# Performance work log

Hardware: AMD Instinct MI355X
Metric: run time of the kernel (lower is better)

## Reference

```python
import math
import jax, jax.numpy as jnp
import numpy as np

C = 1024
H = 16
HD = C // H
T = 2048
B = 2
EPS = 1e-5


def setup_inputs() -> dict:
    key = jax.random.key(0)
    ks = jax.random.split(key, 8)
    s = 0.02
    return {
        "x": jax.random.normal(ks[0], (B, T, C), dtype=jnp.float32),
        "ln1_g": jnp.ones((C,), jnp.float32),
        "ln1_b": jnp.zeros((C,), jnp.float32),
        "w_attn": jax.random.normal(ks[1], (C, 3 * C), dtype=jnp.float32) * s,
        "b_attn": jnp.zeros((3 * C,), jnp.float32),
        "w_proj": jax.random.normal(ks[2], (C, C), dtype=jnp.float32) * s,
        "b_proj": jnp.zeros((C,), jnp.float32),
        "ln2_g": jnp.ones((C,), jnp.float32),
        "ln2_b": jnp.zeros((C,), jnp.float32),
        "w_fc": jax.random.normal(ks[3], (C, 4 * C), dtype=jnp.float32) * s,
        "b_fc": jnp.zeros((4 * C,), jnp.float32),
        "w_fc2": jax.random.normal(ks[4], (4 * C, C), dtype=jnp.float32) * s,
        "b_fc2": jnp.zeros((C,), jnp.float32),
    }


def _layernorm(x, g, b):
    mu = jnp.mean(x, axis=-1, keepdims=True)
    var = jnp.mean((x - mu) ** 2, axis=-1, keepdims=True)
    return (x - mu) * jax.lax.rsqrt(var + EPS) * g + b


def _attention(x, w_attn, b_attn, w_proj, b_proj):
    Bb, Tt, Cc = x.shape
    qkv = x @ w_attn + b_attn  # (B,T,3C)
    q, k, v = jnp.split(qkv, 3, axis=-1)
    # (B,H,T,HD)
    q = q.reshape(Bb, Tt, H, HD).transpose(0, 2, 1, 3)
    k = k.reshape(Bb, Tt, H, HD).transpose(0, 2, 1, 3)
    v = v.reshape(Bb, Tt, H, HD).transpose(0, 2, 1, 3)
    scale = 1.0 / math.sqrt(HD)
    attn = jnp.einsum("bhqd,bhkd->bhqk", q, k) * scale
    causal = jnp.tril(jnp.ones((Tt, Tt), dtype=bool))
    attn = jnp.where(causal[None, None], attn, -jnp.inf)
    attn = jax.nn.softmax(attn, axis=-1)
    out = jnp.einsum("bhqk,bhkd->bhqd", attn, v)
    out = out.transpose(0, 2, 1, 3).reshape(Bb, Tt, Cc)
    return out @ w_proj + b_proj


def _mlp(x, w_fc, b_fc, w_fc2, b_fc2):
    h = jax.nn.gelu(x @ w_fc + b_fc, approximate=True)
    return h @ w_fc2 + b_fc2


def reference(x, ln1_g, ln1_b, w_attn, b_attn, w_proj, b_proj,
              ln2_g, ln2_b, w_fc, b_fc, w_fc2, b_fc2):
    x = x + _attention(_layernorm(x, ln1_g, ln1_b), w_attn, b_attn, w_proj, b_proj)
    x = x + _mlp(_layernorm(x, ln2_g, ln2_b), w_fc, b_fc, w_fc2, b_fc2)
    return x
```

## Files before the change

kernel.cpp:

```cpp
#include <hip/hip_runtime.h>
#include <math.h>

#define TB 2
#define TT 2048
#define TC 1024
#define TH 16
#define THD 64
#define TM (TB*TT)
#define NQT 32

typedef __bf16 bf16x8 __attribute__((ext_vector_type(8)));
typedef float f32x4 __attribute__((ext_vector_type(4)));
typedef unsigned short u16x8 __attribute__((ext_vector_type(8)));
typedef unsigned short u16x4 __attribute__((ext_vector_type(4)));

__device__ __forceinline__ unsigned short f2bf(float f){
    unsigned int u = __builtin_bit_cast(unsigned int, f);
    u = (u + 0x7FFFu + ((u >> 16) & 1u)) >> 16;
    return (unsigned short)u;
}
__device__ __forceinline__ bf16x8 ldbf8(const unsigned short* p){
    return __builtin_bit_cast(bf16x8, *(const u16x8*)p);
}
__device__ __forceinline__ void gl_lds16(const void* g, void* l){
    __builtin_amdgcn_global_load_lds(
        (const __attribute__((address_space(1))) unsigned int*)g,
        (__attribute__((address_space(3))) unsigned int*)l,
        16, 0, 0);
}
__device__ __forceinline__ float gelu_tanh(float v){
    float u = 2.0f * 0.7978845608028654f * (v + 0.044715f * v * v * v);
    u = fminf(fmaxf(u, -30.f), 30.f);
    float e = __expf(u);
    return 0.5f * v * (1.f + (e - 1.f) / (e + 1.f));
}

__global__ __launch_bounds__(256)
void convert_transpose(const float* __restrict__ in, unsigned short* __restrict__ out,
                       int K, int N){
    __shared__ float tile[32][33];
    int tx = threadIdx.x, ty = threadIdx.y;
    int n0 = blockIdx.x * 32, k0 = blockIdx.y * 32;
    #pragma unroll
    for (int i = 0; i < 4; i++)
        tile[ty + 8*i][tx] = in[(size_t)(k0 + ty + 8*i) * N + n0 + tx];
    __syncthreads();
    #pragma unroll
    for (int i = 0; i < 4; i++)
        out[(size_t)(n0 + ty + 8*i) * K + k0 + tx] = f2bf(tile[tx][ty + 8*i]);
}

__global__ __launch_bounds__(256)
void ln_kernel(const float* __restrict__ x, const float* __restrict__ g,
               const float* __restrict__ be, unsigned short* __restrict__ y){
    const int row = blockIdx.x, t = threadIdx.x;
    const float4* xr = (const float4*)(x + (size_t)row * TC);
    float4 v = xr[t];
    float s  = v.x + v.y + v.z + v.w;
    float s2 = v.x*v.x + v.y*v.y + v.z*v.z + v.w*v.w;
    #pragma unroll
    for (int off = 32; off; off >>= 1){
        s  += __shfl_down(s,  off);
        s2 += __shfl_down(s2, off);
    }
    __shared__ float red[8];
    int l = t & 63, wv = t >> 6;
    if (l == 0){ red[wv] = s; red[4 + wv] = s2; }
    __syncthreads();
    float S  = red[0] + red[1] + red[2] + red[3];
    float S2 = red[4] + red[5] + red[6] + red[7];
    float mu = S * (1.f / TC);
    float var = S2 * (1.f / TC) - mu * mu;
    float rs = rsqrtf(var + 1e-5f);
    int c = t * 4;
    float4 gg = *(const float4*)(g + c);
    float4 bb = *(const float4*)(be + c);
    u16x4 o;
    o[0] = f2bf((v.x - mu) * rs * gg.x + bb.x);
    o[1] = f2bf((v.y - mu) * rs * gg.y + bb.y);
    o[2] = f2bf((v.z - mu) * rs * gg.z + bb.z);
    o[3] = f2bf((v.w - mu) * rs * gg.w + bb.w);
    *(u16x4*)(y + (size_t)row * TC + c) = o;
}

template<int EPI>
__global__ __launch_bounds__(256, 2)
void gemm_bt(const unsigned short* __restrict__ A,
             const unsigned short* __restrict__ Bt,
             const float* __restrict__ bias,
             const float* __restrict__ resid,
             void* __restrict__ outv, void* __restrict__ outv2,
             int M, int N, int K, int klen){
    __shared__ unsigned short lA[128 * 32];
    __shared__ unsigned short lB[128 * 32];
    const int t = threadIdx.x, w = t >> 6, l = t & 63, lr = l & 15, lg = l >> 4;
    const int nt = N >> 7;
    const int nwg = gridDim.x;
    const int bid = blockIdx.x;
    int wg = (nwg & 7) ? bid : ((bid & 7) * (nwg >> 3) + (bid >> 3));
    const int ntile = (M >> 7) * nt;
    const int kh = wg / ntile;
    wg -= kh * ntile;
    const int bm = wg / nt, bn = wg % nt;
    const int row0 = bm << 7, col0 = bn << 7;
    const int wr = w >> 1, wc = w & 1;
    const int kbeg = kh * klen, kend = kbeg + klen;

    f32x4 acc[4][4];
    #pragma unroll
    for (int i = 0; i < 4; i++)
        #pragma unroll
        for (int j = 0; j < 4; j++) acc[i][j] = (f32x4){0.f,0.f,0.f,0.f};

    const char* Ag = (const char*)(A + (size_t)(row0 + (t >> 2)) * K) + (t & 3) * 16;
    const char* Bg = (const char*)(Bt + (size_t)(col0 + (t >> 2)) * K) + (t & 3) * 16;
    const size_t rstep = (size_t)64 * K * 2;
    char* lAw = (char*)lA + w * 1024;
    char* lBw = (char*)lB + w * 1024;

    for (int k0 = kbeg; k0 < kend; k0 += 32){
        size_t kb = (size_t)k0 * 2;
        gl_lds16(Ag + kb,          lAw);
        gl_lds16(Ag + kb + rstep,  lAw + 4096);
        gl_lds16(Bg + kb,          lBw);
        gl_lds16(Bg + kb + rstep,  lBw + 4096);
        __syncthreads();
        bf16x8 af[4], bfr[4];
        #pragma unroll
        for (int mi = 0; mi < 4; mi++)
            af[mi] = ldbf8(lA + (wr*64 + mi*16 + lr) * 32 + lg * 8);
        #pragma unroll
        for (int ni = 0; ni < 4; ni++)
            bfr[ni] = ldbf8(lB + (wc*64 + ni*16 + lr) * 32 + lg * 8);
        #pragma unroll
        for (int mi = 0; mi < 4; mi++)
            #pragma unroll
            for (int ni = 0; ni < 4; ni++)
                acc[mi][ni] = __builtin_amdgcn_mfma_f32_16x16x32_bf16(
                    af[mi], bfr[ni], acc[mi][ni], 0, 0, 0);
        __syncthreads();
    }

    float bcol[4];
    #pragma unroll
    for (int ni = 0; ni < 4; ni++)
        bcol[ni] = (EPI == 3) ? 0.f : bias[col0 + wc*64 + ni*16 + lr];
    float* fout = (EPI == 3) ? (kh ? (float*)outv2 : (float*)outv) : (float*)outv;
    #pragma unroll
    for (int mi = 0; mi < 4; mi++){
        #pragma unroll
        for (int j = 0; j < 4; j++){
            int row = row0 + wr*64 + mi*16 + lg*4 + j;
            size_t base = (size_t)row * N + col0 + wc*64 + lr;
            #pragma unroll
            for (int ni = 0; ni < 4; ni++){
                float v = acc[mi][ni][j] + bcol[ni];
                size_t idx = base + (size_t)ni * 16;
                if (EPI == 0)      ((unsigned short*)outv)[idx] = f2bf(v);
                else if (EPI == 1) ((float*)outv)[idx] = v + resid[idx];
                else if (EPI == 2) ((unsigned short*)outv)[idx] = f2bf(gelu_tanh(v));
                else               fout[idx] = v;
            }
        }
    }
}

__global__ __launch_bounds__(256)
void combine_k(const float* __restrict__ p0, const float* __restrict__ p1,
               const float* __restrict__ bias, const float* __restrict__ resid,
               float* __restrict__ out){
    const int total = TM * TC / 4;
    for (int i = blockIdx.x * 256 + threadIdx.x; i < total; i += gridDim.x * 256){
        int e = i * 4;
        float4 a = *(const float4*)(p0 + e);
        float4 b = *(const float4*)(p1 + e);
        float4 r = *(const float4*)(resid + e);
        float4 bb = *(const float4*)(bias + (e & (TC - 1)));
        float4 o;
        o.x = a.x + b.x + r.x + bb.x;
        o.y = a.y + b.y + r.y + bb.y;
        o.z = a.z + b.z + r.z + bb.z;
        o.w = a.w + b.w + r.w + bb.w;
        *(float4*)(out + e) = o;
    }
}

template<int MH>
__device__ __forceinline__ void gloadA(const unsigned short* bufA, bf16x8 (&af)[4][2],
                                       int wm, int lr, int sl0, int sl1){
    #pragma unroll
    for (int i = 0; i < 4; i++){
        int lrow = (wm*128 + (MH*4 + i)*16 + lr) * 64;
        af[i][0] = ldbf8(bufA + lrow + sl0);
        af[i][1] = ldbf8(bufA + lrow + sl1);
    }
}
__device__ __forceinline__ void gloadB(const unsigned short* bufB, bf16x8 (&bfr)[4][2],
                                       int wn, int lr, int sl0, int sl1){
    #pragma unroll
    for (int i = 0; i < 4; i++){
        int brow = (wn*64 + i*16 + lr) * 64;
        bfr[i][0] = ldbf8(bufB + brow + sl0);
        bfr[i][1] = ldbf8(bufB + brow + sl1);
    }
}
template<int MH, int NH>
__device__ __forceinline__ void gmma(const bf16x8 (&af)[4][2], const bf16x8 (&bfr)[4][2],
                                     f32x4 (&acc)[8][4]){
    #pragma unroll
    for (int i = 0; i < 4; i++)
        #pragma unroll
        for (int j = 0; j < 2; j++){
            f32x4& a = acc[MH*4 + i][NH*2 + j];
            a = __builtin_amdgcn_mfma_f32_16x16x32_bf16(af[i][0], bfr[NH*2+j][0], a, 0,0,0);
            a = __builtin_amdgcn_mfma_f32_16x16x32_bf16(af[i][1], bfr[NH*2+j][1], a, 0,0,0);
        }
}

template<int EPI>
__global__ __launch_bounds__(512, 1)
void gemm256(const unsigned short* __restrict__ A,
             const unsigned short* __restrict__ Bt,
             const float* __restrict__ bias,
             void* __restrict__ outv,
             int M, int N, int K){
    __shared__ unsigned short lds[2][2][256*64];
    const int t = threadIdx.x;
    const int w = t >> 6, l = t & 63, lr = l & 15, lg = l >> 4;
    const int wm = w >> 2, wn = w & 3;
    const int lr7 = lr & 7;
    const int sl0 = (lg ^ lr7) << 3;
    const int sl1 = ((4 + lg) ^ lr7) << 3;
    const int nbn = N >> 8;
    const int nwg = (M >> 8) * nbn;
    const int bid = blockIdx.x;
    const int wg = (nwg & 7) ? bid : ((bid & 7) * (nwg >> 3) + (bid >> 3));
    const int bm = wg / nbn, bn = wg % nbn;
    const size_t row0 = (size_t)bm << 8, col0 = (size_t)bn << 8;
    const int NT = K >> 6;

    f32x4 acc[8][4];
    #pragma unroll
    for (int i = 0; i < 8; i++)
        #pragma unroll
        for (int j = 0; j < 4; j++) acc[i][j] = (f32x4){0.f,0.f,0.f,0.f};

    int rowc[4], slogc[4];
    #pragma unroll
    for (int c = 0; c < 4; c++){
        int seg = t + (c << 9);
        rowc[c]  = seg >> 3;
        slogc[c] = (((seg & 7) ^ ((seg >> 3) & 7)) << 3);
    }
    const unsigned short* Abase = A  + row0 * K;
    const unsigned short* Bbase = Bt + col0 * K;
    auto stage = [&](int buf, int kt, int c){
        int seg = t + (c << 9);
        const unsigned short* sa = Abase + (size_t)rowc[c] * K + kt*64 + slogc[c];
        const unsigned short* sb = Bbase + (size_t)rowc[c] * K + kt*64 + slogc[c];
        gl_lds16(sa, (void*)&lds[buf][0][seg * 8]);
        gl_lds16(sb, (void*)&lds[buf][1][seg * 8]);
    };

    #pragma unroll
    for (int c = 0; c < 4; c++) stage(0, 0, c);

    for (int tk = 0; tk < NT; ++tk){
        const int cur = tk & 1;
        const bool more = (tk + 1) < NT;
        const unsigned short* bufA = &lds[cur][0][0];
        const unsigned short* bufB = &lds[cur][1][0];

        if (more){
            stage(cur ^ 1, tk + 1, 0);
            asm volatile("s_waitcnt vmcnt(2)" ::: "memory");
        } else {
            asm volatile("s_waitcnt vmcnt(0)" ::: "memory");
        }
        __builtin_amdgcn_s_barrier();

        bf16x8 af[4][2], bfr[4][2];
        gloadA<0>(bufA, af, wm, lr, sl0, sl1);
        gloadB(bufB, bfr, wn, lr, sl0, sl1);
        if (more) stage(cur ^ 1, tk + 1, 1);
        __builtin_amdgcn_s_barrier();
        asm volatile("s_waitcnt lgkmcnt(0)" ::: "memory");
        __builtin_amdgcn_sched_barrier(0);
        __builtin_amdgcn_s_setprio(1);
        gmma<0,0>(af, bfr, acc);
        __builtin_amdgcn_s_setprio(0);
        __builtin_amdgcn_s_barrier();
        if (more) stage(cur ^ 1, tk + 1, 2);
        __builtin_amdgcn_s_setprio(1);
        gmma<0,1>(af, bfr, acc);
        __builtin_amdgcn_s_setprio(0);
        __builtin_amdgcn_s_barrier();
        gloadA<1>(bufA, af, wm, lr, sl0, sl1);
        if (more) stage(cur ^ 1, tk + 1, 3);
        __builtin_amdgcn_s_barrier();
        asm volatile("s_waitcnt lgkmcnt(0)" ::: "memory");
        __builtin_amdgcn_sched_barrier(0);
        __builtin_amdgcn_s_setprio(1);
        gmma<1,0>(af, bfr, acc);
        __builtin_amdgcn_s_setprio(0);
        __builtin_amdgcn_s_barrier();
        __builtin_amdgcn_s_setprio(1);
        gmma<1,1>(af, bfr, acc);
        __builtin_amdgcn_s_setprio(0);
        __builtin_amdgcn_s_barrier();
    }

    float bcol[4];
    #pragma unroll
    for (int ni = 0; ni < 4; ni++) bcol[ni] = bias[col0 + wn*64 + ni*16 + lr];
    unsigned short* outp = (unsigned short*)outv;
    #pragma unroll
    for (int mi = 0; mi < 8; mi++){
        #pragma unroll
        for (int j = 0; j < 4; j++){
            size_t row = row0 + wm*128 + mi*16 + lg*4 + j;
            size_t base = row * N + col0 + wn*64 + lr;
            #pragma unroll
            for (int ni = 0; ni < 4; ni++){
                float v = acc[mi][ni][j] + bcol[ni];
                size_t idx = base + (size_t)ni * 16;
                if (EPI == 0) outp[idx] = f2bf(v);
                else          outp[idx] = f2bf(gelu_tanh(v));
            }
        }
    }
}

__global__ __launch_bounds__(256)
void vtrans(const unsigned short* __restrict__ qkv, unsigned short* __restrict__ vTg){
    __shared__ unsigned short lt[64][68];
    int kt = blockIdx.x & (NQT - 1);
    int bh = blockIdx.x >> 5;
    int h = bh & (TH - 1), b = bh >> 4;
    int t = threadIdx.x;
    int r = t >> 2, c4 = t & 3;
    const unsigned short* src = qkv + (size_t)(b*TT + kt*64 + r) * (3*TC) + 2*TC + h*THD;
    u16x8 a0 = *(const u16x8*)(src + c4*8);
    u16x8 a1 = *(const u16x8*)(src + 32 + c4*8);
    #pragma unroll
    for (int j = 0; j < 8; j++){
        lt[r][c4*8 + j]      = a0[j];
        lt[r][32 + c4*8 + j] = a1[j];
    }
    __syncthreads();
    int d = t >> 2;
    unsigned short* dst = vTg + ((size_t)bh * NQT + kt) * (64*80) + (size_t)d * 80;
    u16x8 o0, o1;
    #pragma unroll
    for (int j = 0; j < 8; j++){
        o0[j] = lt[c4*8 + j][d];
        o1[j] = lt[32 + c4*8 + j][d];
    }
    *(u16x8*)(dst + c4*8)      = o0;
    *(u16x8*)(dst + 32 + c4*8) = o1;
}

__global__ __launch_bounds__(512, 2)
void attn_kernel(const unsigned short* __restrict__ qkv,
                 const unsigned short* __restrict__ vTg,
                 unsigned short* __restrict__ attn_out){
    __shared__ unsigned short kbuf[2][64*64];
    __shared__ unsigned short vbuf[2][64*64];
    __shared__ unsigned short pl[8][16*72];

    const int bid = blockIdx.x;
    const int qrank = bid >> 5;
    const int bh = bid & 31;
    const int h = bh & (TH - 1), b = bh >> 4;
    const int qb = 15 - qrank;
    const int q0 = qb << 7;
    const int t = threadIdx.x, w = t >> 6, l = t & 63, lr = l & 15, lg = l >> 4;
    const int lr7 = lr & 7;
    const int sl0 = (lg ^ lr7) << 3;
    const int sl1 = ((4 + lg) ^ lr7) << 3;
    const float SC = 0.18033688011112042f;

    const int NKT = 2*qb + 2;
    const int qrow_base = q0 + w*16;
    const int kdiag = qrow_base >> 6;

    const int srow = t >> 3, sslot = t & 7;
    const int scol = (sslot ^ (srow & 7)) * 8;
    const unsigned short* kg =
        qkv + (size_t)(b*TT + srow) * (3*TC) + TC + h*THD + scol;
    const unsigned short* vg =
        vTg + (size_t)bh * (NQT*64*80) + (size_t)srow * 80 + scol;
    const size_t kstep = (size_t)64 * (3*TC);

    auto stage = [&](int kt, int buf){
        gl_lds16(kg + (size_t)kt * kstep,   (void*)&kbuf[buf][t*8]);
        gl_lds16(vg + (size_t)kt * (64*80), (void*)&vbuf[buf][t*8]);
    };

    const unsigned short* qr =
        qkv + (size_t)(b*TT + qrow_base + lr) * (3*TC) + h*THD;
    bf16x8 q0f = ldbf8(qr + lg*8), q1f = ldbf8(qr + 32 + lg*8);

    bf16x8 ones;
    #pragma unroll
    for (int i = 0; i < 8; i++) ones[i] = (__bf16)1.0f;

    f32x4 o[5];
    float m[4];
    #pragma unroll
    for (int i = 0; i < 5; i++) o[i] = (f32x4){0.f,0.f,0.f,0.f};
    #pragma unroll
    for (int i = 0; i < 4; i++) m[i] = -1e30f;

    unsigned short* plw = &pl[w][0];

    stage(0, 0);
    for (int kt = 0; kt < NKT; ++kt){
        const int cur = kt & 1;
        const bool more = (kt + 1) < NKT;
        if (more){
            stage(kt + 1, cur ^ 1);
            asm volatile("s_waitcnt vmcnt(2)" ::: "memory");
        } else {
            asm volatile("s_waitcnt vmcnt(0)" ::: "memory");
        }
        __builtin_amdgcn_s_barrier();

        const unsigned short* kb = &kbuf[cur][0];
        f32x4 s[4];
        __builtin_amdgcn_s_setprio(1);
        #pragma unroll
        for (int cb = 0; cb < 4; cb++){
            bf16x8 ka = ldbf8(kb + (cb*16 + lr)*64 + sl0);
            bf16x8 kbf = ldbf8(kb + (cb*16 + lr)*64 + sl1);
            f32x4 z = (f32x4){0.f,0.f,0.f,0.f};
            z = __builtin_amdgcn_mfma_f32_16x16x32_bf16(q0f, ka, z, 0,0,0);
            z = __builtin_amdgcn_mfma_f32_16x16x32_bf16(q1f, kbf, z, 0,0,0);
            s[cb] = z;
        }
        __builtin_amdgcn_s_setprio(0);
        #pragma unroll
        for (int cb = 0; cb < 4; cb++)
            #pragma unroll
            for (int j = 0; j < 4; j++) s[cb][j] *= SC;
        if (kt >= kdiag){
            #pragma unroll
            for (int cb = 0; cb < 4; cb++)
                #pragma unroll
                for (int j = 0; j < 4; j++)
                    if (kt*64 + cb*16 + lr > qrow_base + lg*4 + j) s[cb][j] = -1e30f;
        }
        float mloc[4];
        #pragma unroll
        for (int j = 0; j < 4; j++)
            mloc[j] = fmaxf(fmaxf(s[0][j], s[1][j]), fmaxf(s[2][j], s[3][j]));
        #pragma unroll
        for (int off = 1; off < 16; off <<= 1)
            #pragma unroll
            for (int j = 0; j < 4; j++)
                mloc[j] = fmaxf(mloc[j], __shfl_xor(mloc[j], off));
        float al[4];
        #pragma unroll
        for (int j = 0; j < 4; j++){
            float mn = fmaxf(m[j], mloc[j]);
            al[j] = exp2f(m[j] - mn);
            m[j] = mn;
        }
        #pragma unroll
        for (int db = 0; db < 5; db++)
            #pragma unroll
            for (int j = 0; j < 4; j++) o[db][j] *= al[j];
        #pragma unroll
        for (int cb = 0; cb < 4; cb++)
            #pragma unroll
            for (int j = 0; j < 4; j++){
                float e = exp2f(s[cb][j] - m[j]);
                ((__bf16*)plw)[(lg*4 + j)*72 + cb*16 + lr] = (__bf16)e;
            }
        const unsigned short* vb = &vbuf[cur][0];
        bf16x8 pa0 = ldbf8(plw + lr*72 + lg*8);
        bf16x8 pa1 = ldbf8(plw + lr*72 + 32 + lg*8);
        __builtin_amdgcn_s_setprio(1);
        #pragma unroll
        for (int db = 0; db < 4; db++){
            bf16x8 va = ldbf8(vb + (db*16 + lr)*64 + sl0);
            bf16x8 vbf = ldbf8(vb + (db*16 + lr)*64 + sl1);
            o[db] = __builtin_amdgcn_mfma_f32_16x16x32_bf16(pa0, va, o[db], 0,0,0);
            o[db] = __builtin_amdgcn_mfma_f32_16x16x32_bf16(pa1, vbf, o[db], 0,0,0);
        }
        o[4] = __builtin_amdgcn_mfma_f32_16x16x32_bf16(pa0, ones, o[4], 0,0,0);
        o[4] = __builtin_amdgcn_mfma_f32_16x16x32_bf16(pa1, ones, o[4], 0,0,0);
        __builtin_amdgcn_s_setprio(0);

        __builtin_amdgcn_s_barrier();
    }

    __bf16* aout = (__bf16*)attn_out;
    #pragma unroll
    for (int j = 0; j < 4; j++){
        float inv = 1.f / o[4][j];
        size_t tok = (size_t)(b*TT + qrow_base + lg*4 + j);
        #pragma unroll
        for (int db = 0; db < 4; db++)
            aout[tok*TC + h*THD + db*16 + lr] = (__bf16)(o[db][j] * inv);
    }
}

extern "C" void kernel_launch(void* const* d_in, const int* in_sizes, int n_in,
                              void* d_out, int out_size, void* d_ws, size_t ws_size,
                              hipStream_t stream){
    const float* x      = (const float*)d_in[0];
    const float* ln1_g  = (const float*)d_in[1];
    const float* ln1_b  = (const float*)d_in[2];
    const float* w_attn = (const float*)d_in[3];
    const float* b_attn = (const float*)d_in[4];
    const float* w_proj = (const float*)d_in[5];
    const float* b_proj = (const float*)d_in[6];
    const float* ln2_g  = (const float*)d_in[7];
    const float* ln2_b  = (const float*)d_in[8];
    const float* w_fc   = (const float*)d_in[9];
    const float* b_fc   = (const float*)d_in[10];
    const float* w_fc2  = (const float*)d_in[11];
    const float* b_fc2  = (const float*)d_in[12];
    float* out = (float*)d_out;

    char* ws = (char*)d_ws;
    size_t off = 0;
    auto alloc = [&](size_t bytes) -> void* {
        void* p = ws + off;
        off += (bytes + 255) & ~(size_t)255;
        return p;
    };
    unsigned short* wattnT = (unsigned short*)alloc((size_t)3072*1024*2);
    unsigned short* wprojT = (unsigned short*)alloc((size_t)1024*1024*2);
    unsigned short* wfcT   = (unsigned short*)alloc((size_t)4096*1024*2);
    unsigned short* wfc2T  = (unsigned short*)alloc((size_t)1024*4096*2);
    unsigned short* xn1    = (unsigned short*)alloc((size_t)TM*TC*2);
    unsigned short* qkvb   = (unsigned short*)alloc((size_t)TM*3*TC*2);
    float*          resid1 = (float*)alloc((size_t)TM*TC*4);
    unsigned short* xn2    = (unsigned short*)alloc((size_t)TM*TC*2);
    unsigned short* hbuf   = (unsigned short*)alloc((size_t)TM*4*TC*2);
    unsigned short* attnO  = (unsigned short*)alloc((size_t)TM*TC*2);
    unsigned short* vTg    = (unsigned short*)alloc((size_t)TB*TH*NQT*64*80*2);

    float* p0 = (float*)qkvb;
    float* p1 = (float*)attnO;

    dim3 tb(32, 8, 1);
    convert_transpose<<<dim3(3072/32, 1024/32), tb, 0, stream>>>(w_attn, wattnT, 1024, 3072);
    convert_transpose<<<dim3(1024/32, 1024/32), tb, 0, stream>>>(w_proj, wprojT, 1024, 1024);
    convert_transpose<<<dim3(4096/32, 1024/32), tb, 0, stream>>>(w_fc,   wfcT,   1024, 4096);
    convert_transpose<<<dim3(1024/32, 4096/32), tb, 0, stream>>>(w_fc2,  wfc2T,  4096, 1024);

    ln_kernel<<<TM, 256, 0, stream>>>(x, ln1_g, ln1_b, xn1);

    gemm256<0><<<(TM/256)*(3072/256), 512, 0, stream>>>(
        xn1, wattnT, b_attn, qkvb, TM, 3072, 1024);

    vtrans<<<TB*TH*NQT, 256, 0, stream>>>(qkvb, vTg);

    attn_kernel<<<TB*TH*(TT/128), 512, 0, stream>>>(qkvb, vTg, attnO);

    gemm_bt<1><<<(TM/128)*(1024/128), 256, 0, stream>>>(
        attnO, wprojT, b_proj, x, resid1, nullptr, TM, 1024, 1024, 1024);

    ln_kernel<<<TM, 256, 0, stream>>>(resid1, ln2_g, ln2_b, xn2);

    gemm256<2><<<(TM/256)*(4096/256), 512, 0, stream>>>(
        xn2, wfcT, b_fc, hbuf, TM, 4096, 1024);

    gemm_bt<3><<<2*(TM/128)*(1024/128), 256, 0, stream>>>(
        hbuf, wfc2T, nullptr, nullptr, p0, p1, TM, 1024, 4096, 2048);
    combine_k<<<2048, 256, 0, stream>>>(p0, p1, b_fc2, resid1, out);
}
```

Baseline: 261.4 us.

## Use 256-tile split-K GEMM for FC2 with bf16 partials, merge weight conversions

The FC2 GEMM moves from the 128-tile two-way split-K kernel with fp32 partials to a new 256-tile, four-way split-K kernel built on the pipelined gemm256 loop. It writes bf16 partials into a reused buffer, and a combine kernel sums them. The four weight convert-transpose launches become one launch, and the attention scale multiply is folded into the exp FMA and the max. The aim is higher MFMA efficiency, less partial-sum traffic and fewer launches, at the cost of rounding the partial sums to bf16.

After: 243.8 us. -6.7%, faster.

```diff
diff --git a/kernel.cpp b/kernel.cpp
--- a/kernel.cpp
+++ b/kernel.cpp
@@ -19,6 +19,10 @@
     u = (u + 0x7FFFu + ((u >> 16) & 1u)) >> 16;
     return (unsigned short)u;
 }
+__device__ __forceinline__ float bf2f(unsigned short h){
+    unsigned int u = ((unsigned int)h) << 16;
+    return __builtin_bit_cast(float, u);
+}
 __device__ __forceinline__ bf16x8 ldbf8(const unsigned short* p){
     return __builtin_bit_cast(bf16x8, *(const u16x8*)p);
 }
@@ -36,11 +40,19 @@
 }
 
 __global__ __launch_bounds__(256)
-void convert_transpose(const float* __restrict__ in, unsigned short* __restrict__ out,
-                       int K, int N){
+void convert_all(const float* __restrict__ w_attn, const float* __restrict__ w_proj,
+                 const float* __restrict__ w_fc,   const float* __restrict__ w_fc2,
+                 unsigned short* __restrict__ wattnT, unsigned short* __restrict__ wprojT,
+                 unsigned short* __restrict__ wfcT,   unsigned short* __restrict__ wfc2T){
     __shared__ float tile[32][33];
+    const int bid = blockIdx.x;
+    const float* in; unsigned short* out; int K, N, bx, by;
+    if (bid < 3072)      { in=w_attn; out=wattnT; K=1024; N=3072; bx=bid%96;  by=bid/96; }
+    else if (bid < 4096) { int lo=bid-3072; in=w_proj; out=wprojT; K=1024; N=1024; bx=lo%32;  by=lo/32; }
+    else if (bid < 8192) { int lo=bid-4096; in=w_fc;   out=wfcT;   K=1024; N=4096; bx=lo%128; by=lo/128; }
+    else                 { int lo=bid-8192; in=w_fc2;  out=wfc2T;  K=4096; N=1024; bx=lo%32;  by=lo/32; }
     int tx = threadIdx.x, ty = threadIdx.y;
-    int n0 = blockIdx.x * 32, k0 = blockIdx.y * 32;
+    int n0 = bx * 32, k0 = by * 32;
     #pragma unroll
     for (int i = 0; i < 4; i++)
         tile[ty + 8*i][tx] = in[(size_t)(k0 + ty + 8*i) * N + n0 + tx];
@@ -89,8 +101,8 @@
              const unsigned short* __restrict__ Bt,
              const float* __restrict__ bias,
              const float* __restrict__ resid,
-             void* __restrict__ outv, void* __restrict__ outv2,
-             int M, int N, int K, int klen){
+             void* __restrict__ outv,
+             int M, int N, int K){
     __shared__ unsigned short lA[128 * 32];
     __shared__ unsigned short lB[128 * 32];
     const int t = threadIdx.x, w = t >> 6, l = t & 63, lr = l & 15, lg = l >> 4;
@@ -98,13 +110,9 @@
     const int nwg = gridDim.x;
     const int bid = blockIdx.x;
     int wg = (nwg & 7) ? bid : ((bid & 7) * (nwg >> 3) + (bid >> 3));
-    const int ntile = (M >> 7) * nt;
-    const int kh = wg / ntile;
-    wg -= kh * ntile;
     const int bm = wg / nt, bn = wg % nt;
     const int row0 = bm << 7, col0 = bn << 7;
     const int wr = w >> 1, wc = w & 1;
-    const int kbeg = kh * klen, kend = kbeg + klen;
 
     f32x4 acc[4][4];
     #pragma unroll
@@ -118,7 +126,7 @@
     char* lAw = (char*)lA + w * 1024;
     char* lBw = (char*)lB + w * 1024;
 
-    for (int k0 = kbeg; k0 < kend; k0 += 32){
+    for (int k0 = 0; k0 < K; k0 += 32){
         size_t kb = (size_t)k0 * 2;
         gl_lds16(Ag + kb,          lAw);
         gl_lds16(Ag + kb + rstep,  lAw + 4096);
@@ -143,9 +151,7 @@
 
     float bcol[4];
     #pragma unroll
-    for (int ni = 0; ni < 4; ni++)
-        bcol[ni] = (EPI == 3) ? 0.f : bias[col0 + wc*64 + ni*16 + lr];
-    float* fout = (EPI == 3) ? (kh ? (float*)outv2 : (float*)outv) : (float*)outv;
+    for (int ni = 0; ni < 4; ni++) bcol[ni] = bias[col0 + wc*64 + ni*16 + lr];
     #pragma unroll
     for (int mi = 0; mi < 4; mi++){
         #pragma unroll
@@ -158,30 +164,9 @@
                 size_t idx = base + (size_t)ni * 16;
                 if (EPI == 0)      ((unsigned short*)outv)[idx] = f2bf(v);
                 else if (EPI == 1) ((float*)outv)[idx] = v + resid[idx];
-                else if (EPI == 2) ((unsigned short*)outv)[idx] = f2bf(gelu_tanh(v));
-                else               fout[idx] = v;
+                else               ((unsigned short*)outv)[idx] = f2bf(gelu_tanh(v));
             }
         }
-    }
-}
-
-__global__ __launch_bounds__(256)
-void combine_k(const float* __restrict__ p0, const float* __restrict__ p1,
-               const float* __restrict__ bias, const float* __restrict__ resid,
-               float* __restrict__ out){
-    const int total = TM * TC / 4;
-    for (int i = blockIdx.x * 256 + threadIdx.x; i < total; i += gridDim.x * 256){
-        int e = i * 4;
-        float4 a = *(const float4*)(p0 + e);
-        float4 b = *(const float4*)(p1 + e);
-        float4 r = *(const float4*)(resid + e);
-        float4 bb = *(const float4*)(bias + (e & (TC - 1)));
-        float4 o;
-        o.x = a.x + b.x + r.x + bb.x;
-        o.y = a.y + b.y + r.y + bb.y;
-        o.z = a.z + b.z + r.z + bb.z;
-        o.w = a.w + b.w + r.w + bb.w;
-        *(float4*)(out + e) = o;
     }
 }
 
@@ -216,6 +201,50 @@
             a = __builtin_amdgcn_mfma_f32_16x16x32_bf16(af[i][1], bfr[NH*2+j][1], a, 0,0,0);
         }
 }
+
+#define G256_LOOP(NT_, KBEG_)                                                   \
+    for (int tk = 0; tk < (NT_); ++tk){                                         \
+        const int cur = tk & 1;                                                 \
+        const bool more = (tk + 1) < (NT_);                                     \
+        const unsigned short* bufA = &lds[cur][0][0];                           \
+        const unsigned short* bufB = &lds[cur][1][0];                           \
+        if (more){                                                              \
+            stage(cur ^ 1, (KBEG_) + (tk + 1)*64, 0);                           \
+            asm volatile("s_waitcnt vmcnt(2)" ::: "memory");                    \
+        } else {                                                                \
+            asm volatile("s_waitcnt vmcnt(0)" ::: "memory");                    \
+        }                                                                       \
+        __builtin_amdgcn_s_barrier();                                           \
+        bf16x8 af[4][2], bfr[4][2];                                             \
+        gloadA<0>(bufA, af, wm, lr, sl0, sl1);                                  \
+        gloadB(bufB, bfr, wn, lr, sl0, sl1);                                    \
+        if (more) stage(cur ^ 1, (KBEG_) + (tk + 1)*64, 1);                     \
+        __builtin_amdgcn_s_barrier();                                           \
+        asm volatile("s_waitcnt lgkmcnt(0)" ::: "memory");                      \
+        __builtin_amdgcn_sched_barrier(0);                                      \
+        __builtin_amdgcn_s_setprio(1);                                          \
+        gmma<0,0>(af, bfr, acc);                                                \
+        __builtin_amdgcn_s_setprio(0);                                          \
+        __builtin_amdgcn_s_barrier();                                           \
+        if (more) stage(cur ^ 1, (KBEG_) + (tk + 1)*64, 2);                     \
+        __builtin_amdgcn_s_setprio(1);                                          \
+        gmma<0,1>(af, bfr, acc);                                                \
+        __builtin_amdgcn_s_setprio(0);                                          \
+        __builtin_amdgcn_s_barrier();                                           \
+        gloadA<1>(bufA, af, wm, lr, sl0, sl1);                                  \
+        if (more) stage(cur ^ 1, (KBEG_) + (tk + 1)*64, 3);                     \
+        __builtin_amdgcn_s_barrier();                                           \
+        asm volatile("s_waitcnt lgkmcnt(0)" ::: "memory");                      \
+        __builtin_amdgcn_sched_barrier(0);                                      \
+        __builtin_amdgcn_s_setprio(1);                                          \
+        gmma<1,0>(af, bfr, acc);                                                \
+        __builtin_amdgcn_s_setprio(0);                                          \
+        __builtin_amdgcn_s_barrier();                                           \
+        __builtin_amdgcn_s_setprio(1);                                          \
+        gmma<1,1>(af, bfr, acc);                                                \
+        __builtin_amdgcn_s_setprio(0);                                          \
+        __builtin_amdgcn_s_barrier();                                           \
+    }
 
 template<int EPI>
 __global__ __launch_bounds__(512, 1)
@@ -254,10 +283,10 @@
     }
     const unsigned short* Abase = A  + row0 * K;
     const unsigned short* Bbase = Bt + col0 * K;
-    auto stage = [&](int buf, int kt, int c){
+    auto stage = [&](int buf, int kofs, int c){
         int seg = t + (c << 9);
-        const unsigned short* sa = Abase + (size_t)rowc[c] * K + kt*64 + slogc[c];
-        const unsigned short* sb = Bbase + (size_t)rowc[c] * K + kt*64 + slogc[c];
+        const unsigned short* sa = Abase + (size_t)rowc[c] * K + kofs + slogc[c];
+        const unsigned short* sb = Bbase + (size_t)rowc[c] * K + kofs + slogc[c];
         gl_lds16(sa, (void*)&lds[buf][0][seg * 8]);
         gl_lds16(sb, (void*)&lds[buf][1][seg * 8]);
     };
@@ -265,50 +294,7 @@
     #pragma unroll
     for (int c = 0; c < 4; c++) stage(0, 0, c);
 
-    for (int tk = 0; tk < NT; ++tk){
-        const int cur = tk & 1;
-        const bool more = (tk + 1) < NT;
-        const unsigned short* bufA = &lds[cur][0][0];
-        const unsigned short* bufB = &lds[cur][1][0];
-
-        if (more){
-            stage(cur ^ 1, tk + 1, 0);
-            asm volatile("s_waitcnt vmcnt(2)" ::: "memory");
-        } else {
-            asm volatile("s_waitcnt vmcnt(0)" ::: "memory");
-        }
-        __builtin_amdgcn_s_barrier();
-
-        bf16x8 af[4][2], bfr[4][2];
-        gloadA<0>(bufA, af, wm, lr, sl0, sl1);
-        gloadB(bufB, bfr, wn, lr, sl0, sl1);
-        if (more) stage(cur ^ 1, tk + 1, 1);
-        __builtin_amdgcn_s_barrier();
-        asm volatile("s_waitcnt lgkmcnt(0)" ::: "memory");
-        __builtin_amdgcn_sched_barrier(0);
-        __builtin_amdgcn_s_setprio(1);
-        gmma<0,0>(af, bfr, acc);
-        __builtin_amdgcn_s_setprio(0);
-        __builtin_amdgcn_s_barrier();
-        if (more) stage(cur ^ 1, tk + 1, 2);
-        __builtin_amdgcn_s_setprio(1);
-        gmma<0,1>(af, bfr, acc);
-        __builtin_amdgcn_s_setprio(0);
-        __builtin_amdgcn_s_barrier();
-        gloadA<1>(bufA, af, wm, lr, sl0, sl1);
-        if (more) stage(cur ^ 1, tk + 1, 3);
-        __builtin_amdgcn_s_barrier();
-        asm volatile("s_waitcnt lgkmcnt(0)" ::: "memory");
-        __builtin_amdgcn_sched_barrier(0);
-        __builtin_amdgcn_s_setprio(1);
-        gmma<1,0>(af, bfr, acc);
-        __builtin_amdgcn_s_setprio(0);
-        __builtin_amdgcn_s_barrier();
-        __builtin_amdgcn_s_setprio(1);
-        gmma<1,1>(af, bfr, acc);
-        __builtin_amdgcn_s_setprio(0);
-        __builtin_amdgcn_s_barrier();
-    }
+    G256_LOOP(NT, 0)
 
     float bcol[4];
     #pragma unroll
@@ -328,6 +314,95 @@
                 else          outp[idx] = f2bf(gelu_tanh(v));
             }
         }
+    }
+}
+
+__global__ __launch_bounds__(512, 1)
+void gemm256sk(const unsigned short* __restrict__ A,
+               const unsigned short* __restrict__ Bt,
+               unsigned short* __restrict__ pout,
+               int M, int N, int K, int klen){
+    __shared__ unsigned short lds[2][2][256*64];
+    const int t = threadIdx.x;
+    const int w = t >> 6, l = t & 63, lr = l & 15, lg = l >> 4;
+    const int wm = w >> 2, wn = w & 3;
+    const int lr7 = lr & 7;
+    const int sl0 = (lg ^ lr7) << 3;
+    const int sl1 = ((4 + lg) ^ lr7) << 3;
+    const int nbn = N >> 8;
+    const int ntile = (M >> 8) * nbn;
+    const int nwg = gridDim.x;
+    const int bid = blockIdx.x;
+    int wg = (nwg & 7) ? bid : ((bid & 7) * (nwg >> 3) + (bid >> 3));
+    const int kh = wg / ntile;
+    wg -= kh * ntile;
+    const int bm = wg / nbn, bn = wg % nbn;
+    const size_t row0 = (size_t)bm << 8, col0 = (size_t)bn << 8;
+    const int NT = klen >> 6;
+    const int kbeg = kh * klen;
+
+    f32x4 acc[8][4];
+    #pragma unroll
+    for (int i = 0; i < 8; i++)
+        #pragma unroll
+        for (int j = 0; j < 4; j++) acc[i][j] = (f32x4){0.f,0.f,0.f,0.f};
+
+    int rowc[4], slogc[4];
+    #pragma unroll
+    for (int c = 0; c < 4; c++){
+        int seg = t + (c << 9);
+        rowc[c]  = seg >> 3;
+        slogc[c] = (((seg & 7) ^ ((seg >> 3) & 7)) << 3);
+    }
+    const unsigned short* Abase = A  + row0 * K;
+    const unsigned short* Bbase = Bt + col0 * K;
+    auto stage = [&](int buf, int kofs, int c){
+        int seg = t + (c << 9);
+        const unsigned short* sa = Abase + (size_t)rowc[c] * K + kofs + slogc[c];
+        const unsigned short* sb = Bbase + (size_t)rowc[c] * K + kofs + slogc[c];
+        gl_lds16(sa, (void*)&lds[buf][0][seg * 8]);
+        gl_lds16(sb, (void*)&lds[buf][1][seg * 8]);
+    };
+
+    #pragma unroll
+    for (int c = 0; c < 4; c++) stage(0, kbeg, c);
+
+    G256_LOOP(NT, kbeg)
+
+    unsigned short* outp = pout + (size_t)kh * M * N;
+    #pragma unroll
+    for (int mi = 0; mi < 8; mi++){
+        #pragma unroll
+        for (int j = 0; j < 4; j++){
+            size_t row = row0 + wm*128 + mi*16 + lg*4 + j;
+            size_t base = row * N + col0 + wn*64 + lr;
+            #pragma unroll
+            for (int ni = 0; ni < 4; ni++)
+                outp[base + (size_t)ni * 16] = f2bf(acc[mi][ni][j]);
+        }
+    }
+}
+
+__global__ __launch_bounds__(256)
+void combine_k4(const unsigned short* __restrict__ p,
+                const float* __restrict__ bias, const float* __restrict__ resid,
+                float* __restrict__ out){
+    const size_t PS = (size_t)TM * TC;
+    const int total = TM * TC / 4;
+    for (int i = blockIdx.x * 256 + threadIdx.x; i < total; i += gridDim.x * 256){
+        int e = i * 4;
+        u16x4 a0 = *(const u16x4*)(p + e);
+        u16x4 a1 = *(const u16x4*)(p + PS + e);
+        u16x4 a2 = *(const u16x4*)(p + 2*PS + e);
+        u16x4 a3 = *(const u16x4*)(p + 3*PS + e);
+        float4 r = *(const float4*)(resid + e);
+        float4 bb = *(const float4*)(bias + (e & (TC - 1)));
+        float4 o;
+        o.x = bf2f(a0[0]) + bf2f(a1[0]) + bf2f(a2[0]) + bf2f(a3[0]) + r.x + bb.x;
+        o.y = bf2f(a0[1]) + bf2f(a1[1]) + bf2f(a2[1]) + bf2f(a3[1]) + r.y + bb.y;
+        o.z = bf2f(a0[2]) + bf2f(a1[2]) + bf2f(a2[2]) + bf2f(a3[2]) + r.z + bb.z;
+        o.w = bf2f(a0[3]) + bf2f(a1[3]) + bf2f(a2[3]) + bf2f(a3[3]) + r.w + bb.w;
+        *(float4*)(out + e) = o;
     }
 }
 
@@ -439,10 +514,6 @@
             s[cb] = z;
         }
         __builtin_amdgcn_s_setprio(0);
-        #pragma unroll
-        for (int cb = 0; cb < 4; cb++)
-            #pragma unroll
-            for (int j = 0; j < 4; j++) s[cb][j] *= SC;
         if (kt >= kdiag){
             #pragma unroll
             for (int cb = 0; cb < 4; cb++)
@@ -462,7 +533,7 @@
         float al[4];
         #pragma unroll
         for (int j = 0; j < 4; j++){
-            float mn = fmaxf(m[j], mloc[j]);
+            float mn = fmaxf(m[j], mloc[j] * SC);
             al[j] = exp2f(m[j] - mn);
             m[j] = mn;
         }
@@ -474,7 +545,7 @@
         for (int cb = 0; cb < 4; cb++)
             #pragma unroll
             for (int j = 0; j < 4; j++){
-                float e = exp2f(s[cb][j] - m[j]);
+                float e = exp2f(__builtin_fmaf(s[cb][j], SC, -m[j]));
                 ((__bf16*)plw)[(lg*4 + j)*72 + cb*16 + lr] = (__bf16)e;
             }
         const unsigned short* vb = &vbuf[cur][0];
@@ -543,14 +614,10 @@
     unsigned short* attnO  = (unsigned short*)alloc((size_t)TM*TC*2);
     unsigned short* vTg    = (unsigned short*)alloc((size_t)TB*TH*NQT*64*80*2);
 
-    float* p0 = (float*)qkvb;
-    float* p1 = (float*)attnO;
-
-    dim3 tb(32, 8, 1);
-    convert_transpose<<<dim3(3072/32, 1024/32), tb, 0, stream>>>(w_attn, wattnT, 1024, 3072);
-    convert_transpose<<<dim3(1024/32, 1024/32), tb, 0, stream>>>(w_proj, wprojT, 1024, 1024);
-    convert_transpose<<<dim3(4096/32, 1024/32), tb, 0, stream>>>(w_fc,   wfcT,   1024, 4096);
-    convert_transpose<<<dim3(1024/32, 4096/32), tb, 0, stream>>>(w_fc2,  wfc2T,  4096, 1024);
+    unsigned short* pks = xn1;
+
+    convert_all<<<12288, dim3(32, 8, 1), 0, stream>>>(
+        w_attn, w_proj, w_fc, w_fc2, wattnT, wprojT, wfcT, wfc2T);
 
     ln_kernel<<<TM, 256, 0, stream>>>(x, ln1_g, ln1_b, xn1);
 
@@ -562,14 +629,14 @@
     attn_kernel<<<TB*TH*(TT/128), 512, 0, stream>>>(qkvb, vTg, attnO);
 
     gemm_bt<1><<<(TM/128)*(1024/128), 256, 0, stream>>>(
-        attnO, wprojT, b_proj, x, resid1, nullptr, TM, 1024, 1024, 1024);
+        attnO, wprojT, b_proj, x, resid1, TM, 1024, 1024);
 
     ln_kernel<<<TM, 256, 0, stream>>>(resid1, ln2_g, ln2_b, xn2);
 
     gemm256<2><<<(TM/256)*(4096/256), 512, 0, stream>>>(
         xn2, wfcT, b_fc, hbuf, TM, 4096, 1024);
 
-    gemm_bt<3><<<2*(TM/128)*(1024/128), 256, 0, stream>>>(
-        hbuf, wfc2T, nullptr, nullptr, p0, p1, TM, 1024, 4096, 2048);
-    combine_k<<<2048, 256, 0, stream>>>(p0, p1, b_fc2, resid1, out);
-}
+    gemm256sk<<<4*(TM/256)*(1024/256), 512, 0, stream>>>(
+        hbuf, wfc2T, pks, TM, 1024, 4096, 1024);
+    combine_k4<<<2048, 256, 0, stream>>>(pks, b_fc2, resid1, out);
+}
```
